# Kernel tuning notes

Measured on AMD Instinct MI355X. Metric: run time of the kernel, lower is better.

Reference implementation:

```python
import jax, jax.numpy as jnp
import numpy as np

B, S, E, F, C, V = 4, 2048, 100, 64, 8922, 52000

def _conv1d_same(x, w, b, k):
    # x: [B,E,S], w: [F,E,k] -> [B,F,S] with 'same' padding (floor(k/2))
    out = jax.lax.conv_general_dilated(
        x, w, window_strides=(1,), padding=[(k // 2, k // 2)],
        dimension_numbers=('NCH', 'OIH', 'NCH'))
    return out + b[None, :, None]

def setup_inputs() -> dict:
    key = jax.random.key(0)
    ks = jax.random.split(key, 18)
    sc = 0.05
    inp = {
        'x': jax.random.randint(ks[0], (B, S), 0, V),
        'y': (jax.random.uniform(ks[1], (B, C)) < 0.3).astype(jnp.float32),
        'embed': jax.random.normal(ks[2], (V, E), dtype=jnp.float32) * 0.02,
        'w3': jax.random.normal(ks[3], (F, E, 3), dtype=jnp.float32) * sc,
        'b3': jnp.zeros((F,), jnp.float32),
        'w5': jax.random.normal(ks[4], (F, E, 5), dtype=jnp.float32) * sc,
        'b5': jnp.zeros((F,), jnp.float32),
        'w7': jax.random.normal(ks[5], (F, E, 7), dtype=jnp.float32) * sc,
        'b7': jnp.zeros((F,), jnp.float32),
        'w9': jax.random.normal(ks[6], (F, E, 9), dtype=jnp.float32) * sc,
        'b9': jnp.zeros((F,), jnp.float32),
        'U3': jax.random.normal(ks[7], (C, F), dtype=jnp.float32) * sc,
        'U5': jax.random.normal(ks[8], (C, F), dtype=jnp.float32) * sc,
        'U7': jax.random.normal(ks[9], (C, F), dtype=jnp.float32) * sc,
        'U9': jax.random.normal(ks[10], (C, F), dtype=jnp.float32) * sc,
        'Wf': jax.random.normal(ks[11], (C, 4 * F), dtype=jnp.float32) * sc,
        'bf': jnp.zeros((C,), jnp.float32),
    }
    return inp

def reference(x, y, embed, w3, b3, w5, b5, w7, b7, w9, b9, U3, U5, U7, U9, Wf, bf):
    xe = embed[x]                 # [B,S,E] (dropout is identity at inference)
    xt = xe.transpose(0, 2, 1)    # [B,E,S]

    def branch(w, b, U, k):
        h = jnp.tanh(_conv1d_same(xt, w, b, k)).transpose(0, 2, 1)  # [B,S,F]
        scores = jnp.einsum('cf,bsf->bcs', U, h)                    # [B,C,S]
        alpha = jax.nn.softmax(scores, axis=2)
        return jnp.einsum('bcs,bsf->bcf', alpha, h)                 # [B,C,F]

    m = jnp.concatenate([branch(w3, b3, U3, 3), branch(w5, b5, U5, 5),
                         branch(w7, b7, U7, 7), branch(w9, b9, U9, 9)], axis=2)  # [B,C,4F]
    y_hat = jnp.sum(Wf * m, axis=2) + bf                             # [B,C]
    # binary_cross_entropy_with_logits, mean reduction
    loss = jnp.mean(jnp.maximum(y_hat, 0.0) - y_hat * y + jnp.log1p(jnp.exp(-jnp.abs(y_hat))))
    return (y_hat, loss)
```

## Files before the change

### kernel.cpp

```cpp
#include <hip/hip_runtime.h>
#include <hip/hip_bf16.h>

#define B_ 4
#define S_ 2048
#define E_ 100
#define F_ 64
#define C_ 8922
#define V_ 52000

typedef short bf16x8 __attribute__((ext_vector_type(8)));
typedef short s16x4  __attribute__((ext_vector_type(4)));
typedef float f32x4  __attribute__((ext_vector_type(4)));

#define MFMA16(A, B, C) __builtin_amdgcn_mfma_f32_16x16x32_bf16(A, B, C, 0, 0, 0)
#define LOG2E 1.44269504088896f
#define EXP2F(x) __builtin_amdgcn_exp2f(x)

__device__ inline short bfb(float x) {
    __hip_bfloat16 h = __float2bfloat16(x);
    return *reinterpret_cast<short*>(&h);
}

__global__ __launch_bounds__(256) void prep_kernel(
    const float* __restrict__ w3, const float* __restrict__ w5,
    const float* __restrict__ w7, const float* __restrict__ w9,
    unsigned short* __restrict__ Wp,
    float* __restrict__ num, float* __restrict__ den)
{
    const int gid = blockIdx.x * 256 + threadIdx.x;
    if (gid < 4 * B_ * C_) { num[gid] = 0.f; den[gid] = 0.f; }

    const int j    = gid & 7;
    const int lane = (gid >> 3) & 63;
    const int nt   = (gid >> 9) & 15;
    const int step = gid >> 13;
    const int d    = step >> 2;
    const int ec   = step & 3;
    const int g    = lane >> 4;
    const int lr   = lane & 15;
    const int k    = g * 4 + (j & 3) + ((j >> 2) << 4);
    const int e    = ec * 32 + k;
    const int n    = nt * 16 + lr;
    const int br   = n >> 6;
    const int f    = n & 63;
    const int kb   = 3 + 2 * br;
    const int dp   = d - (3 - br);

    float val = 0.f;
    if (e < E_ && dp >= 0 && dp < kb) {
        const float* w = (br == 0) ? w3 : (br == 1) ? w5 : (br == 2) ? w7 : w9;
        val = w[((size_t)f * E_ + e) * kb + dp];
    }
    Wp[gid] = (unsigned short)bfb(val);
}


__global__ __launch_bounds__(256, 2) void conv_mfma_kernel(
    const int* __restrict__ x, const float* __restrict__ embed,
    const unsigned short* __restrict__ Wp,
    const float* __restrict__ b3, const float* __restrict__ b5,
    const float* __restrict__ b7, const float* __restrict__ b9,
    char* __restrict__ hkB, char* __restrict__ hvB)
{
    __shared__ unsigned short xeT[24 * 128];
    __shared__ float ep[4][16][68];

    const int blk  = blockIdx.x;
    const int b    = blk >> 7;
    const int st   = blk & 127;
    const int s0   = st * 16;
    const int tid  = threadIdx.x;
    const int wave = tid >> 6;
    const int lane = tid & 63;
    const int g    = lane >> 4;
    const int lr   = lane & 15;

    for (int task = tid; task < 384; task += 256) {
        const int row = task >> 4;
        const int o   = task & 15;
        const int s   = s0 - 4 + row;
        float v[8];
        #pragma unroll
        for (int i = 0; i < 8; ++i) v[i] = 0.f;
        if (s >= 0 && s < S_ && o < 13) {
            const int tok = x[b * S_ + s];
            const float* er = embed + (size_t)tok * E_ + o * 8;
            if (o < 12) {
                #pragma unroll
                for (int i = 0; i < 8; ++i) v[i] = er[i];
            } else {
                v[0] = er[0]; v[1] = er[1]; v[2] = er[2]; v[3] = er[3];
            }
        }
        unsigned short u[8];
        #pragma unroll
        for (int i = 0; i < 8; ++i) u[i] = (unsigned short)bfb(v[i]);
        const unsigned xr = ((unsigned)(row & 15)) << 3;
        char* base = (char*)xeT + row * 256;
        *(uint2*)(base + (((unsigned)(o * 16)) ^ xr))     = *(const uint2*)&u[0];
        *(uint2*)(base + (((unsigned)(o * 16 + 8)) ^ xr)) = *(const uint2*)&u[4];
    }
    __syncthreads();

    f32x4 acc[4];
    #pragma unroll
    for (int ns = 0; ns < 4; ++ns) acc[ns] = (f32x4){0.f, 0.f, 0.f, 0.f};

    const char* xb = (const char*)xeT;
    #pragma unroll
    for (int step = 0; step < 36; ++step) {
        const int d  = step >> 2;
        const int ec = step & 3;

        bf16x8 Af;
        {
            const int row = lr + d;
            const unsigned xr = ((unsigned)(row & 15)) << 3;
            const unsigned rb = (unsigned)row * 256;
            const unsigned e0 = (unsigned)(ec * 64 + g * 8);
            const s16x4 lo = *(const s16x4*)(xb + rb + (e0 ^ xr));
            const s16x4 hi = *(const s16x4*)(xb + rb + ((e0 + 32) ^ xr));
            Af = __builtin_shufflevector(lo, hi, 0, 1, 2, 3, 4, 5, 6, 7);
        }

        bf16x8 Bf[4];
        #pragma unroll
        for (int ns = 0; ns < 4; ++ns)
            Bf[ns] = *(const bf16x8*)(Wp +
                     (((size_t)step * 16 + wave * 4 + ns) * 64 + lane) * 8);

        #pragma unroll
        for (int ns = 0; ns < 4; ++ns)
            acc[ns] = MFMA16(Af, Bf[ns], acc[ns]);
    }

    const float* bias = (wave == 0) ? b3 : (wave == 1) ? b5 : (wave == 2) ? b7 : b9;
    float bia[4];
    #pragma unroll
    for (int ns = 0; ns < 4; ++ns) bia[ns] = bias[ns * 16 + lr];

    #pragma unroll
    for (int ns = 0; ns < 4; ++ns)
        #pragma unroll
        for (int r = 0; r < 4; ++r)
            ep[wave][4 * g + r][ns * 16 + lr] = tanhf(acc[ns][r] + bia[ns]);
    __syncthreads();

    const size_t hbase = (size_t)(wave * 4 + b) * 262144;
    #pragma unroll
    for (int it = 0; it < 2; ++it) {
        const int task = it * 64 + lane;
        const int sl = task >> 3;
        const int o  = task & 7;
        const int s  = s0 + sl;
        float v[8];
        *(float4*)&v[0] = *(const float4*)&ep[wave][sl][o * 8];
        *(float4*)&v[4] = *(const float4*)&ep[wave][sl][o * 8 + 4];
        unsigned short u[8];
        #pragma unroll
        for (int i = 0; i < 8; ++i) u[i] = (unsigned short)bfb(v[i]);
        uint4 pk;
        pk.x = (unsigned)u[0] | ((unsigned)u[1] << 16);
        pk.y = (unsigned)u[2] | ((unsigned)u[3] << 16);
        pk.z = (unsigned)u[4] | ((unsigned)u[5] << 16);
        pk.w = (unsigned)u[6] | ((unsigned)u[7] << 16);
        char* hka = hkB + hbase + (size_t)s * 128 +
                    (((unsigned)(o * 16)) ^ (((unsigned)(s & 7)) << 4));
        *(uint4*)hka = pk;
        char* hva = hvB + hbase + (size_t)(s >> 5) * 4096 + (o >> 1) * 1024 +
                    ((s >> 4) & 1) * 512 + ((s >> 2) & 3) * 128 +
                    (s & 3) * 32 + (o & 1) * 16;
        *(uint4*)hva = pk;
    }
}

#define TRREAD(dst, off) \
    asm volatile("ds_read_b64_tr_b16 %0, %1 offset:" #off \
                 : "=v"(dst) : "v"(vaddr));

typedef const __attribute__((address_space(1))) unsigned int* as1_u32p;
typedef __attribute__((address_space(3))) unsigned int* as3_u32p;

__device__ inline void gl_lds16(const void* g, unsigned lds_off) {
    __builtin_amdgcn_global_load_lds((as1_u32p)(uintptr_t)g,
                                     (as3_u32p)(uintptr_t)lds_off, 16, 0, 0);
}

__global__ __launch_bounds__(256, 2) void attn_mfma_kernel(
    const float* __restrict__ U3, const float* __restrict__ U5,
    const float* __restrict__ U7, const float* __restrict__ U9,
    const char* __restrict__ hkG, const char* __restrict__ hvG,
    const float* __restrict__ Wf,
    float* __restrict__ num, float* __restrict__ den)
{
    __shared__ unsigned short Kbuf[2][4096];
    __shared__ unsigned short Vbuf[2][4096];

    const int tid  = threadIdx.x;
    const int wave = tid >> 6;
    const int lane = tid & 63;
    const int g    = lane >> 4;
    const int lr   = lane & 15;

    const int bid  = blockIdx.x;
    const int xcd  = bid & 7;
    const int t2   = bid >> 3;
    const int grp  = xcd + 8 * (t2 / 70);
    const int rest = t2 % 70;
    const int ct   = rest % 35;
    const int sc   = rest / 35;
    const int br   = grp >> 2;
    const int b    = grp & 3;
    const int c0   = ct * 256 + wave * 64;
    const int cb0  = sc * 16;

    const float* __restrict__ U =
        (br == 0) ? U3 : (br == 1) ? U5 : (br == 2) ? U7 : U9;

    bf16x8 Qf[4][2];
    #pragma unroll
    for (int cs = 0; cs < 4; ++cs) {
        int c = c0 + cs * 16 + lr;
        if (c > C_ - 1) c = C_ - 1;
        const float* Uc = U + (size_t)c * F_;
        #pragma unroll
        for (int kh = 0; kh < 2; ++kh) {
            const float4 lo = *(const float4*)(Uc + kh * 32 + g * 8);
            const float4 hi = *(const float4*)(Uc + kh * 32 + g * 8 + 4);
            bf16x8 q;
            q[0] = bfb(lo.x * LOG2E); q[1] = bfb(lo.y * LOG2E);
            q[2] = bfb(lo.z * LOG2E); q[3] = bfb(lo.w * LOG2E);
            q[4] = bfb(hi.x * LOG2E); q[5] = bfb(hi.y * LOG2E);
            q[6] = bfb(hi.z * LOG2E); q[7] = bfb(hi.w * LOG2E);
            Qf[cs][kh] = q;
        }
    }

    f32x4 acc[4][4];
    #pragma unroll
    for (int cs = 0; cs < 4; ++cs)
        #pragma unroll
        for (int fs = 0; fs < 4; ++fs)
            acc[cs][fs] = (f32x4){0.f, 0.f, 0.f, 0.f};
    float lsum[4] = {0.f, 0.f, 0.f, 0.f};

    const char* hkB = hkG + (size_t)grp * 262144;
    const char* hvB = hvG + (size_t)grp * 262144;
    const unsigned kL0 = (unsigned)(uintptr_t)&Kbuf[0][0];
    const unsigned vL0 = (unsigned)(uintptr_t)&Vbuf[0][0];

#define STAGEKV(chunk, buf) {                                              \
        const size_t go = (size_t)(chunk) * 8192 + wave * 2048 +           \
                          (size_t)(lane << 4);                             \
        const unsigned lo = (unsigned)((buf) * 8192 + wave * 2048);        \
        gl_lds16(hkB + go,        kL0 + lo);                               \
        gl_lds16(hkB + go + 1024, kL0 + lo + 1024);                        \
        gl_lds16(hvB + go,        vL0 + lo);                               \
        gl_lds16(hvB + go + 1024, vL0 + lo + 1024); }

    STAGEKV(cb0, 0)
    __syncthreads();

    const unsigned ksw = ((unsigned)(lr & 7)) << 4;

    for (int t = 0; t < 16; ++t) {
        const int cur = t & 1;
        if (t < 15) STAGEKV(cb0 + t + 1, cur ^ 1)

        const char* Kb = (const char*)Kbuf + cur * 8192;
        bf16x8 Kf[4][2];
        #pragma unroll
        for (int sh = 0; sh < 4; ++sh) {
            const unsigned rowb = (unsigned)((16 * sh + lr) * 128);
            #pragma unroll
            for (int kh = 0; kh < 2; ++kh)
                Kf[sh][kh] = *(const bf16x8*)(
                    Kb + rowb + (((unsigned)(kh * 64 + g * 16)) ^ ksw));
        }

        bf16x8 Pf[4][2];
        #pragma unroll
        for (int cs = 0; cs < 4; ++cs) {
            f32x4 d0 = (f32x4){0.f,0.f,0.f,0.f}, d1 = d0, d2 = d0, d3 = d0;
            __builtin_amdgcn_s_setprio(1);
            d0 = MFMA16(Kf[0][0], Qf[cs][0], d0);
            d0 = MFMA16(Kf[0][1], Qf[cs][1], d0);
            d1 = MFMA16(Kf[1][0], Qf[cs][0], d1);
            d1 = MFMA16(Kf[1][1], Qf[cs][1], d1);
            d2 = MFMA16(Kf[2][0], Qf[cs][0], d2);
            d2 = MFMA16(Kf[2][1], Qf[cs][1], d2);
            d3 = MFMA16(Kf[3][0], Qf[cs][0], d3);
            d3 = MFMA16(Kf[3][1], Qf[cs][1], d3);
            __builtin_amdgcn_s_setprio(0);
            float p[16];
            #pragma unroll
            for (int r = 0; r < 4; ++r) {
                p[r]      = EXP2F(d0[r]);
                p[4 + r]  = EXP2F(d1[r]);
                p[8 + r]  = EXP2F(d2[r]);
                p[12 + r] = EXP2F(d3[r]);
            }
            float sm = 0.f;
            #pragma unroll
            for (int r = 0; r < 16; ++r) sm += p[r];
            lsum[cs] += sm;
            bf16x8 pf0, pf1;
            #pragma unroll
            for (int r = 0; r < 8; ++r) { pf0[r] = bfb(p[r]); pf1[r] = bfb(p[8 + r]); }
            Pf[cs][0] = pf0;
            Pf[cs][1] = pf1;
        }

        const unsigned vaddr = vL0 + (unsigned)(cur * 8192 + g * 128 + lr * 2);
#define PVBLK(fs, O0, O1, O2, O3)                                          \
        {                                                                  \
            s16x4 a0, a1, b0, b1;                                          \
            TRREAD(a0, O0) TRREAD(a1, O1) TRREAD(b0, O2) TRREAD(b1, O3)    \
            asm volatile("s_waitcnt lgkmcnt(0)" ::: "memory");             \
            __builtin_amdgcn_sched_barrier(0);                             \
            const bf16x8 V0 = __builtin_shufflevector(a0, a1, 0,1,2,3,4,5,6,7); \
            const bf16x8 V1 = __builtin_shufflevector(b0, b1, 0,1,2,3,4,5,6,7); \
            __builtin_amdgcn_s_setprio(1);                                 \
            _Pragma("unroll")                                              \
            for (int cs = 0; cs < 4; ++cs) {                               \
                acc[cs][fs] = MFMA16(Pf[cs][0], V0, acc[cs][fs]);          \
                acc[cs][fs] = MFMA16(Pf[cs][1], V1, acc[cs][fs]);          \
            }                                                              \
            __builtin_amdgcn_s_setprio(0);                                 \
        }
        PVBLK(0,    0,  512, 4096, 4608)
        PVBLK(1, 1024, 1536, 5120, 5632)
        PVBLK(2, 2048, 2560, 6144, 6656)
        PVBLK(3, 3072, 3584, 7168, 7680)

        __syncthreads();
    }

    #pragma unroll
    for (int cs = 0; cs < 4; ++cs) {
        lsum[cs] += __shfl_xor(lsum[cs], 16);
        lsum[cs] += __shfl_xor(lsum[cs], 32);
        if (g == 0) {
            const int cden = c0 + cs * 16 + lr;
            if (cden < C_)
                atomicAdd(&den[(size_t)grp * C_ + cden], lsum[cs]);
        }
    }

    #pragma unroll
    for (int cs = 0; cs < 4; ++cs) {
        #pragma unroll
        for (int r = 0; r < 4; ++r) {
            const int cc = c0 + cs * 16 + 4 * g + r;
            const int c  = (cc < C_) ? cc : (C_ - 1);
            const float* wrow = Wf + (size_t)c * (4 * F_) + br * F_ + lr;
            float p = 0.f;
            #pragma unroll
            for (int fs = 0; fs < 4; ++fs)
                p += acc[cs][fs][r] * wrow[fs * 16];
            p += __shfl_xor(p, 1);
            p += __shfl_xor(p, 2);
            p += __shfl_xor(p, 4);
            p += __shfl_xor(p, 8);
            if (lr == 0 && cc < C_)
                atomicAdd(&num[(size_t)grp * C_ + cc], p);
        }
    }
}

__global__ __launch_bounds__(256) void bce_kernel(
    const float* __restrict__ num, const float* __restrict__ den,
    const float* __restrict__ bf, const float* __restrict__ y,
    float* __restrict__ out, float* __restrict__ partials)
{
    const int p = blockIdx.x * 256 + threadIdx.x;
    float bce = 0.f;
    if (p < B_ * C_) {
        const int b = p / C_;
        const int c = p - b * C_;
        float yh = bf[c];
        #pragma unroll
        for (int br = 0; br < 4; ++br) {
            const size_t i = (size_t)(br * 4 + b) * C_ + c;
            yh += num[i] / den[i];
        }
        out[p] = yh;
        bce = fmaxf(yh, 0.f) - yh * y[p] + log1pf(expf(-fabsf(yh)));
    }
    __shared__ float red[256];
    red[threadIdx.x] = bce;
    __syncthreads();
    #pragma unroll
    for (int stp = 128; stp > 0; stp >>= 1) {
        if (threadIdx.x < stp) red[threadIdx.x] += red[threadIdx.x + stp];
        __syncthreads();
    }
    if (threadIdx.x == 0) partials[blockIdx.x] = red[0];
}

__global__ __launch_bounds__(256) void loss_kernel(
    const float* __restrict__ partials, int n, float* __restrict__ out_loss)
{
    __shared__ float red[256];
    float v = (threadIdx.x < n) ? partials[threadIdx.x] : 0.f;
    red[threadIdx.x] = v;
    __syncthreads();
    #pragma unroll
    for (int stp = 128; stp > 0; stp >>= 1) {
        if (threadIdx.x < stp) red[threadIdx.x] += red[threadIdx.x + stp];
        __syncthreads();
    }
    if (threadIdx.x == 0) *out_loss = red[0] / (float)(B_ * C_);
}

extern "C" void kernel_launch(void* const* d_in, const int* in_sizes, int n_in,
                              void* d_out, int out_size, void* d_ws, size_t ws_size,
                              hipStream_t stream)
{
    const int*   x     = (const int*)  d_in[0];
    const float* y     = (const float*)d_in[1];
    const float* embed = (const float*)d_in[2];
    const float* w3    = (const float*)d_in[3];
    const float* b3    = (const float*)d_in[4];
    const float* w5    = (const float*)d_in[5];
    const float* b5    = (const float*)d_in[6];
    const float* w7    = (const float*)d_in[7];
    const float* b7    = (const float*)d_in[8];
    const float* w9    = (const float*)d_in[9];
    const float* b9    = (const float*)d_in[10];
    const float* U3    = (const float*)d_in[11];
    const float* U5    = (const float*)d_in[12];
    const float* U7    = (const float*)d_in[13];
    const float* U9    = (const float*)d_in[14];
    const float* Wf    = (const float*)d_in[15];
    const float* bfv   = (const float*)d_in[16];

    char* wsb = (char*)d_ws;
    float*          num      = (float*)wsb;
    float*          den      = (float*)(wsb + 571008);
    float*          partials = (float*)(wsb + 1142016);
    unsigned short* Wp       = (unsigned short*)(wsb + 1142592);
    char*           hkB      = wsb + 1732608;
    char*           hvB      = wsb + 1732608 + 4194304;
    float*          out      = (float*)d_out;

    prep_kernel<<<1152, 256, 0, stream>>>(w3, w5, w7, w9, Wp, num, den);

    conv_mfma_kernel<<<512, 256, 0, stream>>>(
        x, embed, Wp, b3, b5, b7, b9, hkB, hvB);

    attn_mfma_kernel<<<1120, 256, 0, stream>>>(U3, U5, U7, U9, hkB, hvB, Wf,
                                               num, den);

    const int nblk = (B_ * C_ + 255) / 256;
    bce_kernel<<<nblk, 256, 0, stream>>>(num, den, bfv, y, out, partials);
    loss_kernel<<<1, 256, 0, stream>>>(partials, nblk, out + B_ * C_);
}
```

Baseline: 225.9 us.

## Double-buffer conv MFMA operands, pipeline PV LDS reads, fuse loss reduction

The conv MFMA loop now software-pipelines its A and B fragment loads two steps deep, so the next step's global and LDS loads are issued before the current step's MFMAs. In the attention PV stage, transposed LDS reads are prefetched one block ahead with partial lgkmcnt waits instead of a full wait per block. The separate loss kernel is removed: BCE blocks atomically accumulate into a scalar, and the last block, found with an atomic counter, writes the mean. This saves one launch but makes the loss sum order nondeterministic and raises register pressure.

```diff
diff --git a/kernel.cpp b/kernel.cpp
--- a/kernel.cpp
+++ b/kernel.cpp
@@ -25,10 +25,12 @@
     const float* __restrict__ w3, const float* __restrict__ w5,
     const float* __restrict__ w7, const float* __restrict__ w9,
     unsigned short* __restrict__ Wp,
-    float* __restrict__ num, float* __restrict__ den)
+    float* __restrict__ num, float* __restrict__ den,
+    float* __restrict__ lossAcc, int* __restrict__ counter)
 {
     const int gid = blockIdx.x * 256 + threadIdx.x;
     if (gid < 4 * B_ * C_) { num[gid] = 0.f; den[gid] = 0.f; }
+    if (gid == 0) { *lossAcc = 0.f; *counter = 0; }
 
     const int j    = gid & 7;
     const int lane = (gid >> 3) & 63;
@@ -107,31 +109,43 @@
     for (int ns = 0; ns < 4; ++ns) acc[ns] = (f32x4){0.f, 0.f, 0.f, 0.f};
 
     const char* xb = (const char*)xeT;
-    #pragma unroll
-    for (int step = 0; step < 36; ++step) {
-        const int d  = step >> 2;
-        const int ec = step & 3;
-
-        bf16x8 Af;
-        {
-            const int row = lr + d;
-            const unsigned xr = ((unsigned)(row & 15)) << 3;
-            const unsigned rb = (unsigned)row * 256;
-            const unsigned e0 = (unsigned)(ec * 64 + g * 8);
-            const s16x4 lo = *(const s16x4*)(xb + rb + (e0 ^ xr));
-            const s16x4 hi = *(const s16x4*)(xb + rb + ((e0 + 32) ^ xr));
-            Af = __builtin_shufflevector(lo, hi, 0, 1, 2, 3, 4, 5, 6, 7);
-        }
-
-        bf16x8 Bf[4];
-        #pragma unroll
-        for (int ns = 0; ns < 4; ++ns)
-            Bf[ns] = *(const bf16x8*)(Wp +
-                     (((size_t)step * 16 + wave * 4 + ns) * 64 + lane) * 8);
-
-        #pragma unroll
-        for (int ns = 0; ns < 4; ++ns)
-            acc[ns] = MFMA16(Af, Bf[ns], acc[ns]);
+    const unsigned short* wpb = Wp + ((size_t)wave * 4) * 512 + lane * 8;
+
+#define LOADB(v0, v1, v2, v3, stepv) {                                     \
+        const unsigned short* wp = wpb + (size_t)(stepv) * 8192;           \
+        v0 = *(const bf16x8*)(wp);        v1 = *(const bf16x8*)(wp + 512); \
+        v2 = *(const bf16x8*)(wp + 1024); v3 = *(const bf16x8*)(wp + 1536); }
+
+#define AFLOAD(Afv, stepv) {                                               \
+        const int row = lr + ((stepv) >> 2);                               \
+        const unsigned xr = ((unsigned)(row & 15)) << 3;                   \
+        const unsigned rb = (unsigned)row * 256;                           \
+        const unsigned e0 = (unsigned)((((stepv) & 3)) * 64 + g * 8);      \
+        const s16x4 lo = *(const s16x4*)(xb + rb + (e0 ^ xr));             \
+        const s16x4 hi = *(const s16x4*)(xb + rb + ((e0 + 32) ^ xr));      \
+        Afv = __builtin_shufflevector(lo, hi, 0, 1, 2, 3, 4, 5, 6, 7); }
+
+    bf16x8 A0, A1;
+    bf16x8 B00, B01, B02, B03, B10, B11, B12, B13;
+    LOADB(B00, B01, B02, B03, 0)
+    AFLOAD(A0, 0)
+
+    #pragma unroll
+    for (int sp = 0; sp < 36; sp += 2) {
+        LOADB(B10, B11, B12, B13, sp + 1)
+        AFLOAD(A1, sp + 1)
+        acc[0] = MFMA16(A0, B00, acc[0]);
+        acc[1] = MFMA16(A0, B01, acc[1]);
+        acc[2] = MFMA16(A0, B02, acc[2]);
+        acc[3] = MFMA16(A0, B03, acc[3]);
+        if (sp < 34) {
+            LOADB(B00, B01, B02, B03, sp + 2)
+            AFLOAD(A0, sp + 2)
+        }
+        acc[0] = MFMA16(A1, B10, acc[0]);
+        acc[1] = MFMA16(A1, B11, acc[1]);
+        acc[2] = MFMA16(A1, B12, acc[2]);
+        acc[3] = MFMA16(A1, B13, acc[3]);
     }
 
     const float* bias = (wave == 0) ? b3 : (wave == 1) ? b5 : (wave == 2) ? b7 : b9;
@@ -312,26 +326,66 @@
         }
 
         const unsigned vaddr = vL0 + (unsigned)(cur * 8192 + g * 128 + lr * 2);
-#define PVBLK(fs, O0, O1, O2, O3)                                          \
-        {                                                                  \
-            s16x4 a0, a1, b0, b1;                                          \
-            TRREAD(a0, O0) TRREAD(a1, O1) TRREAD(b0, O2) TRREAD(b1, O3)    \
-            asm volatile("s_waitcnt lgkmcnt(0)" ::: "memory");             \
-            __builtin_amdgcn_sched_barrier(0);                             \
-            const bf16x8 V0 = __builtin_shufflevector(a0, a1, 0,1,2,3,4,5,6,7); \
-            const bf16x8 V1 = __builtin_shufflevector(b0, b1, 0,1,2,3,4,5,6,7); \
-            __builtin_amdgcn_s_setprio(1);                                 \
-            _Pragma("unroll")                                              \
-            for (int cs = 0; cs < 4; ++cs) {                               \
-                acc[cs][fs] = MFMA16(Pf[cs][0], V0, acc[cs][fs]);          \
-                acc[cs][fs] = MFMA16(Pf[cs][1], V1, acc[cs][fs]);          \
-            }                                                              \
-            __builtin_amdgcn_s_setprio(0);                                 \
-        }
-        PVBLK(0,    0,  512, 4096, 4608)
-        PVBLK(1, 1024, 1536, 5120, 5632)
-        PVBLK(2, 2048, 2560, 6144, 6656)
-        PVBLK(3, 3072, 3584, 7168, 7680)
+        {
+            s16x4 pa, pb, pc, pd, qa, qb, qc, qd;
+            __builtin_amdgcn_sched_barrier(0);
+            TRREAD(pa, 0)    TRREAD(pb, 512)  TRREAD(pc, 4096) TRREAD(pd, 4608)
+            TRREAD(qa, 1024) TRREAD(qb, 1536) TRREAD(qc, 5120) TRREAD(qd, 5632)
+            asm volatile("s_waitcnt lgkmcnt(4)" ::: "memory");
+            __builtin_amdgcn_sched_barrier(0);
+            {
+                const bf16x8 V0 = __builtin_shufflevector(pa, pb, 0,1,2,3,4,5,6,7);
+                const bf16x8 V1 = __builtin_shufflevector(pc, pd, 0,1,2,3,4,5,6,7);
+                __builtin_amdgcn_s_setprio(1);
+                #pragma unroll
+                for (int cs = 0; cs < 4; ++cs) {
+                    acc[cs][0] = MFMA16(Pf[cs][0], V0, acc[cs][0]);
+                    acc[cs][0] = MFMA16(Pf[cs][1], V1, acc[cs][0]);
+                }
+                __builtin_amdgcn_s_setprio(0);
+            }
+            TRREAD(pa, 2048) TRREAD(pb, 2560) TRREAD(pc, 6144) TRREAD(pd, 6656)
+            asm volatile("s_waitcnt lgkmcnt(4)" ::: "memory");
+            __builtin_amdgcn_sched_barrier(0);
+            {
+                const bf16x8 V0 = __builtin_shufflevector(qa, qb, 0,1,2,3,4,5,6,7);
+                const bf16x8 V1 = __builtin_shufflevector(qc, qd, 0,1,2,3,4,5,6,7);
+                __builtin_amdgcn_s_setprio(1);
+                #pragma unroll
+                for (int cs = 0; cs < 4; ++cs) {
+                    acc[cs][1] = MFMA16(Pf[cs][0], V0, acc[cs][1]);
+                    acc[cs][1] = MFMA16(Pf[cs][1], V1, acc[cs][1]);
+                }
+                __builtin_amdgcn_s_setprio(0);
+            }
+            TRREAD(qa, 3072) TRREAD(qb, 3584) TRREAD(qc, 7168) TRREAD(qd, 7680)
+            asm volatile("s_waitcnt lgkmcnt(4)" ::: "memory");
+            __builtin_amdgcn_sched_barrier(0);
+            {
+                const bf16x8 V0 = __builtin_shufflevector(pa, pb, 0,1,2,3,4,5,6,7);
+                const bf16x8 V1 = __builtin_shufflevector(pc, pd, 0,1,2,3,4,5,6,7);
+                __builtin_amdgcn_s_setprio(1);
+                #pragma unroll
+                for (int cs = 0; cs < 4; ++cs) {
+                    acc[cs][2] = MFMA16(Pf[cs][0], V0, acc[cs][2]);
+                    acc[cs][2] = MFMA16(Pf[cs][1], V1, acc[cs][2]);
+                }
+                __builtin_amdgcn_s_setprio(0);
+            }
+            asm volatile("s_waitcnt lgkmcnt(0)" ::: "memory");
+            __builtin_amdgcn_sched_barrier(0);
+            {
+                const bf16x8 V0 = __builtin_shufflevector(qa, qb, 0,1,2,3,4,5,6,7);
+                const bf16x8 V1 = __builtin_shufflevector(qc, qd, 0,1,2,3,4,5,6,7);
+                __builtin_amdgcn_s_setprio(1);
+                #pragma unroll
+                for (int cs = 0; cs < 4; ++cs) {
+                    acc[cs][3] = MFMA16(Pf[cs][0], V0, acc[cs][3]);
+                    acc[cs][3] = MFMA16(Pf[cs][1], V1, acc[cs][3]);
+                }
+                __builtin_amdgcn_s_setprio(0);
+            }
+        }
 
         __syncthreads();
     }
@@ -371,7 +425,8 @@
 __global__ __launch_bounds__(256) void bce_kernel(
     const float* __restrict__ num, const float* __restrict__ den,
     const float* __restrict__ bf, const float* __restrict__ y,
-    float* __restrict__ out, float* __restrict__ partials)
+    float* __restrict__ out, float* __restrict__ lossAcc,
+    int* __restrict__ counter)
 {
     const int p = blockIdx.x * 256 + threadIdx.x;
     float bce = 0.f;
@@ -395,22 +450,16 @@
         if (threadIdx.x < stp) red[threadIdx.x] += red[threadIdx.x + stp];
         __syncthreads();
     }
-    if (threadIdx.x == 0) partials[blockIdx.x] = red[0];
-}
-
-__global__ __launch_bounds__(256) void loss_kernel(
-    const float* __restrict__ partials, int n, float* __restrict__ out_loss)
-{
-    __shared__ float red[256];
-    float v = (threadIdx.x < n) ? partials[threadIdx.x] : 0.f;
-    red[threadIdx.x] = v;
-    __syncthreads();
-    #pragma unroll
-    for (int stp = 128; stp > 0; stp >>= 1) {
-        if (threadIdx.x < stp) red[threadIdx.x] += red[threadIdx.x + stp];
-        __syncthreads();
-    }
-    if (threadIdx.x == 0) *out_loss = red[0] / (float)(B_ * C_);
+    if (threadIdx.x == 0) {
+        atomicAdd(lossAcc, red[0]);
+        __threadfence();
+        const int done = atomicAdd(counter, 1);
+        if (done == (int)gridDim.x - 1) {
+            __threadfence();
+            const float total = atomicAdd(lossAcc, 0.f);
+            out[B_ * C_] = total / (float)(B_ * C_);
+        }
+    }
 }
 
 extern "C" void kernel_launch(void* const* d_in, const int* in_sizes, int n_in,
@@ -438,13 +487,15 @@
     char* wsb = (char*)d_ws;
     float*          num      = (float*)wsb;
     float*          den      = (float*)(wsb + 571008);
-    float*          partials = (float*)(wsb + 1142016);
+    float*          lossAcc  = (float*)(wsb + 1142016);
+    int*            counter  = (int*)  (wsb + 1142020);
     unsigned short* Wp       = (unsigned short*)(wsb + 1142592);
     char*           hkB      = wsb + 1732608;
     char*           hvB      = wsb + 1732608 + 4194304;
     float*          out      = (float*)d_out;
 
-    prep_kernel<<<1152, 256, 0, stream>>>(w3, w5, w7, w9, Wp, num, den);
+    prep_kernel<<<1152, 256, 0, stream>>>(w3, w5, w7, w9, Wp, num, den,
+                                          lossAcc, counter);
 
     conv_mfma_kernel<<<512, 256, 0, stream>>>(
         x, embed, Wp, b3, b5, b7, b9, hkB, hvB);
@@ -453,6 +504,6 @@
                                                num, den);
 
     const int nblk = (B_ * C_ + 255) / 256;
-    bce_kernel<<<nblk, 256, 0, stream>>>(num, den, bfv, y, out, partials);
-    loss_kernel<<<1, 256, 0, stream>>>(partials, nblk, out + B_ * C_);
-}
+    bce_kernel<<<nblk, 256, 0, stream>>>(num, den, bfv, y, out,
+                                         lossAcc, counter);
+}
```

Measured after the change: 224.3 us. Within noise of the previous version (-0.7%).
